# Optimization experiments

Measured on AMD Instinct MI355X. Metric: run time of the kernel, lower is better.

The kernel has to match this reference:

```python
import jax, jax.numpy as jnp
import numpy as np

B, S, D_MODEL, D_SPACE = 4, 2048, 1024, 64
N_POOL = 2048  # size of each of the 5 pools (fqk, fv, rqk, rv, knowledge)
TOP_K = 8


def setup_inputs() -> dict:
    key = jax.random.key(0)
    k1, k2, k3 = jax.random.split(key, 3)
    x = jax.random.normal(k1, (B, S, D_MODEL), dtype=jnp.float32)
    W_all = jax.random.normal(k2, (D_MODEL, 6 * D_SPACE), dtype=jnp.float32) * 0.02
    b_all = jnp.zeros((6 * D_SPACE,), dtype=jnp.float32)
    neuron_emb = jax.random.normal(k3, (5 * N_POOL, D_SPACE), dtype=jnp.float32) * 0.02
    return {"x": x, "W_all": W_all, "b_all": b_all, "neuron_emb": neuron_emb}


def _topk_sparsify(w, k):
    # per-token top-k scatter + renormalize (matches torch scatter_ of topk vals)
    b, s, n = w.shape
    flat = w.reshape(b * s, n)
    vals, idx = jax.lax.top_k(flat, k)                      # [BS, k]
    rows = jnp.arange(b * s)[:, None]
    sparse = jnp.zeros_like(flat).at[rows, idx].set(vals)
    sparse = sparse / (sparse.sum(-1, keepdims=True) + 1e-8)
    return sparse.reshape(b, s, n)


def reference(x, W_all, b_all, neuron_emb):
    # F.normalize(neuron_emb, dim=-1)
    norm = jnp.maximum(jnp.linalg.norm(neuron_emb, axis=-1, keepdims=True), 1e-12)
    emb = neuron_emb / norm

    # proj_all: Linear(d_model, 6*d_space); eval mode -> dropout is identity
    proj = jnp.einsum('bsd,de->bse', x, W_all) + b_all      # [B,S,6*d_space]
    h = jnp.split(proj, 6, axis=-1)

    fqk_emb = emb[0 * N_POOL:1 * N_POOL]
    fv_emb = emb[1 * N_POOL:2 * N_POOL]
    rqk_emb = emb[2 * N_POOL:3 * N_POOL]
    rv_emb = emb[3 * N_POOL:4 * N_POOL]
    pool = [fqk_emb, fqk_emb, fv_emb, rqk_emb, rqk_emb, rv_emb]

    outs = []
    for hp, e in zip(h, pool):
        logits = jnp.einsum('bsd,nd->bsn', hp, e)           # [B,S,N_POOL]
        pref = jax.nn.softmax(logits, axis=-1)
        outs.append(_topk_sparsify(pref, TOP_K))
    # (fqk_Q, fqk_K, fv, rqk_Q, rqk_K, rv) stacked: [6,B,S,N_POOL]
    return jnp.stack(outs, axis=0)
```

## Files before the change

kernel.cpp:

```cpp
#include <hip/hip_runtime.h>
#include <hip/hip_bf16.h>
#include <math.h>

#define HEADS   6
#define DMODEL  1024
#define NPROJ   384
#define DSP     64
#define NPOOL   2048
#define NROWS   8192
#define TILE_M  64
#define KT      64
#define KEEP    16

#define LOG2E_F 1.44269504088896340f
#define LOG2E_D 1.4426950408889634
#define C2      14.4269504088896340f

#define NINF (-__builtin_inff())
#define IMAX 0x7fffffff

typedef __attribute__((ext_vector_type(8))) short  short8;
typedef __attribute__((ext_vector_type(4))) float  f32x4;
typedef __attribute__((ext_vector_type(4))) double f64x4;

__device__ __forceinline__ bool bet_d(double v, int vi, double w, int wi) {
    return (v > w) || (v == w && vi < wi);
}
__device__ __forceinline__ unsigned short f2bf(float f) {
    unsigned int u = __float_as_uint(f);
    return (unsigned short)((u + 0x7fffu + ((u >> 16) & 1u)) >> 16);
}
__device__ __forceinline__ float bf2f(unsigned short s) {
    return __uint_as_float(((unsigned int)s) << 16);
}
__device__ __forceinline__ unsigned int packbf2(float a, float b) {
    return (unsigned int)f2bf(a) | ((unsigned int)f2bf(b) << 16);
}

#define DECL8P(r) \
    unsigned tp##r##0=0u,tp##r##1=0u,tp##r##2=0u,tp##r##3=0u, \
             tp##r##4=0u,tp##r##5=0u,tp##r##6=0u,tp##r##7=0u;

#define CSWP(r,hi,lo) { const unsigned a_=tp##r##hi, b_=tp##r##lo; \
    tp##r##hi = a_>b_?a_:b_; tp##r##lo = a_>b_?b_:a_; }

#define INS8P(r,P) \
    if ((P) > tp##r##7) { tp##r##7=(P); \
        CSWP(r,6,7) CSWP(r,5,6) CSWP(r,4,5) CSWP(r,3,4) \
        CSWP(r,2,3) CSWP(r,1,2) CSWP(r,0,1) }

#define TOURNP(r, ROW) { \
    unsigned slot_ = 0u; \
    for (int k_=0;k_<16;++k_) { \
        const unsigned my0_ = tp##r##0; \
        unsigned v_ = my0_; \
        { const unsigned o_=(unsigned)__shfl_xor((int)v_,1,64); v_ = v_>o_?v_:o_; } \
        { const unsigned o_=(unsigned)__shfl_xor((int)v_,2,64); v_ = v_>o_?v_:o_; } \
        { const unsigned o_=(unsigned)__shfl_xor((int)v_,4,64); v_ = v_>o_?v_:o_; } \
        { const unsigned o_=(unsigned)__shfl_xor((int)v_,8,64); v_ = v_>o_?v_:o_; } \
        const bool won_ = (v_ == my0_); \
        tp##r##0 = won_?tp##r##1:tp##r##0; \
        tp##r##1 = won_?tp##r##2:tp##r##1; \
        tp##r##2 = won_?tp##r##3:tp##r##2; \
        tp##r##3 = won_?tp##r##4:tp##r##3; \
        tp##r##4 = won_?tp##r##5:tp##r##4; \
        tp##r##5 = won_?tp##r##6:tp##r##5; \
        tp##r##6 = won_?tp##r##7:tp##r##6; \
        tp##r##7 = won_?0u:tp##r##7; \
        slot_ = (m==k_)?v_:slot_; \
    } \
    ridx16[(ROW)*16 + m] = 2047 - (int)(slot_ & 0x7FFu); }

#define CSWD(hi,lo) { \
    const bool sw_ = bet_d(dv##lo,di##lo,dv##hi,di##hi); \
    const double td_ = dv##hi; const int tj_ = di##hi; \
    dv##hi = sw_?dv##lo:dv##hi; di##hi = sw_?di##lo:di##hi; \
    dv##lo = sw_?td_:dv##lo;    di##lo = sw_?tj_:di##lo; }

#define INS8D(W,CI) \
    if (bet_d(W,CI,dv7,di7)) { dv7=(W); di7=(CI); \
        CSWD(6,7) CSWD(5,6) CSWD(4,5) CSWD(3,4) CSWD(2,3) CSWD(1,2) CSWD(0,1) }

__global__ __launch_bounds__(256)
void prep_k(const float* __restrict__ emb, ushort* __restrict__ ebf)
{
    const int row = blockIdx.x*256 + threadIdx.x;
    const float* src = emb + (size_t)row*DSP;
    float ss = 0.f;
    #pragma unroll
    for (int g=0; g<16; ++g) {
        const float4 v = *(const float4*)(src + g*4);
        ss += v.x*v.x + v.y*v.y + v.z*v.z + v.w*v.w;
    }
    const float inv = LOG2E_F / fmaxf(sqrtf(ss), 1e-12f);
    ushort* dst = ebf + (size_t)row*DSP;
    #pragma unroll
    for (int g=0; g<8; ++g) {
        const float4 a = *(const float4*)(src + g*8);
        const float4 b = *(const float4*)(src + g*8 + 4);
        uint4 o;
        o.x = packbf2(a.x*inv, a.y*inv);
        o.y = packbf2(a.z*inv, a.w*inv);
        o.z = packbf2(b.x*inv, b.y*inv);
        o.w = packbf2(b.z*inv, b.w*inv);
        *(uint4*)(dst + g*8) = o;
    }
}

__global__ __launch_bounds__(256, 3)
void proj_k(const float* __restrict__ x, const float* __restrict__ Wm,
            const float* __restrict__ bb, float* __restrict__ out)
{
    __shared__ __align__(16) float x_t[64*68];
    __shared__ __align__(16) float w_t[64*68];

    const int t    = threadIdx.x;
    const int lane = t & 63;
    const int wv   = t >> 6;
    const int m    = lane & 15;
    const int q    = lane >> 4;
    const int head = blockIdx.y;
    const int row0 = blockIdx.x * TILE_M;
    const size_t obase = ((size_t)head*NROWS + row0) * (size_t)NPOOL;

    int pr0,pr1,pr2,pr3, pc0,pc1,pc2,pc3;
    {
        const f64x4 zz = {0.,0.,0.,0.};
        const f64x4 dpr = __builtin_amdgcn_mfma_f64_16x16x4f64((double)m, 1.0, zz, 0, 0, 0);
        const f64x4 dpc = __builtin_amdgcn_mfma_f64_16x16x4f64(1.0, (double)m, zz, 0, 0, 0);
        pr0=(int)(dpr[0]*0.25+0.5); pr1=(int)(dpr[1]*0.25+0.5);
        pr2=(int)(dpr[2]*0.25+0.5); pr3=(int)(dpr[3]*0.25+0.5);
        pc0=(int)(dpc[0]*0.25+0.5); pc1=(int)(dpc[1]*0.25+0.5);
        pc2=(int)(dpc[2]*0.25+0.5); pc3=(int)(dpc[3]*0.25+0.5);
    }

    f64x4 acc0 = {0.,0.,0.,0.}, acc1 = {0.,0.,0.,0.},
          acc2 = {0.,0.,0.,0.}, acc3 = {0.,0.,0.,0.};

    const int xr = t >> 2;
    const int xq = t & 3;
    const int wr = t >> 4;
    const int cg = t & 15;
    const float* wbase = Wm + head*64 + cg*4;

    float4 xv0,xv1,xv2,xv3, wv0,wv1,wv2,wv3;
    {
        const float* xsrc = x + (size_t)(row0+xr)*DMODEL + xq*16;
        xv0 = *(const float4*)(xsrc);     xv1 = *(const float4*)(xsrc + 4);
        xv2 = *(const float4*)(xsrc + 8); xv3 = *(const float4*)(xsrc + 12);
        wv0 = *(const float4*)(wbase + (size_t)(wr     )*NPROJ);
        wv1 = *(const float4*)(wbase + (size_t)(wr + 16)*NPROJ);
        wv2 = *(const float4*)(wbase + (size_t)(wr + 32)*NPROJ);
        wv3 = *(const float4*)(wbase + (size_t)(wr + 48)*NPROJ);
    }

    for (int kk = 0; kk < DMODEL; kk += KT) {
        __syncthreads();
        {
            const int k0 = xq*16;
            x_t[(k0+ 0)*68+xr]=xv0.x; x_t[(k0+ 1)*68+xr]=xv0.y; x_t[(k0+ 2)*68+xr]=xv0.z; x_t[(k0+ 3)*68+xr]=xv0.w;
            x_t[(k0+ 4)*68+xr]=xv1.x; x_t[(k0+ 5)*68+xr]=xv1.y; x_t[(k0+ 6)*68+xr]=xv1.z; x_t[(k0+ 7)*68+xr]=xv1.w;
            x_t[(k0+ 8)*68+xr]=xv2.x; x_t[(k0+ 9)*68+xr]=xv2.y; x_t[(k0+10)*68+xr]=xv2.z; x_t[(k0+11)*68+xr]=xv2.w;
            x_t[(k0+12)*68+xr]=xv3.x; x_t[(k0+13)*68+xr]=xv3.y; x_t[(k0+14)*68+xr]=xv3.z; x_t[(k0+15)*68+xr]=xv3.w;
            *(float4*)&w_t[(wr     )*68 + cg*4] = wv0;
            *(float4*)&w_t[(wr + 16)*68 + cg*4] = wv1;
            *(float4*)&w_t[(wr + 32)*68 + cg*4] = wv2;
            *(float4*)&w_t[(wr + 48)*68 + cg*4] = wv3;
        }
        __syncthreads();
        if (kk + KT < DMODEL) {
            const float* xsrc = x + (size_t)(row0+xr)*DMODEL + (kk+KT) + xq*16;
            xv0 = *(const float4*)(xsrc);     xv1 = *(const float4*)(xsrc + 4);
            xv2 = *(const float4*)(xsrc + 8); xv3 = *(const float4*)(xsrc + 12);
            wv0 = *(const float4*)(wbase + (size_t)(kk+KT + wr     )*NPROJ);
            wv1 = *(const float4*)(wbase + (size_t)(kk+KT + wr + 16)*NPROJ);
            wv2 = *(const float4*)(wbase + (size_t)(kk+KT + wr + 32)*NPROJ);
            wv3 = *(const float4*)(wbase + (size_t)(kk+KT + wr + 48)*NPROJ);
        }
        #pragma unroll 4
        for (int kq = 0; kq < 16; ++kq) {
            const int kb = kq*4 + q;
            const double a  = (double)x_t[kb*68 + wv*16 + m];
            const double b0 = (double)w_t[kb*68 +      m];
            const double b1 = (double)w_t[kb*68 + 16 + m];
            const double b2 = (double)w_t[kb*68 + 32 + m];
            const double b3 = (double)w_t[kb*68 + 48 + m];
            acc0 = __builtin_amdgcn_mfma_f64_16x16x4f64(a, b0, acc0, 0, 0, 0);
            acc1 = __builtin_amdgcn_mfma_f64_16x16x4f64(a, b1, acc1, 0, 0, 0);
            acc2 = __builtin_amdgcn_mfma_f64_16x16x4f64(a, b2, acc2, 0, 0, 0);
            acc3 = __builtin_amdgcn_mfma_f64_16x16x4f64(a, b3, acc3, 0, 0, 0);
        }
    }

    float*  hhi = out + obase;
    ushort* hlo = (ushort*)(out + obase + 4096);
    const float* bbp = bb + head*64;
    #pragma unroll
    for (int ct = 0; ct < 4; ++ct) {
        const f64x4 a4 = (ct==0)?acc0:(ct==1)?acc1:(ct==2)?acc2:acc3;
        #define WRB(r) { \
            const int row = wv*16 + pr##r; \
            const int col = ct*16 + pc##r; \
            const double v = a4[r] + (double)bbp[col]; \
            const float hi = (float)v; \
            hhi[(size_t)row*64 + col] = hi; \
            hlo[(size_t)row*64 + col] = f2bf((float)(v - (double)hi)); }
        WRB(0) WRB(1) WRB(2) WRB(3)
        #undef WRB
    }
}

__global__ __launch_bounds__(256, 3)
void route_k(const float* __restrict__ emb, const ushort* __restrict__ ebf,
             float* __restrict__ out)
{
    __shared__ int    ridx16[64*16];
    __shared__ float  zbuf[64];
    __shared__ double rv[64*17];
    __shared__ __align__(8) float final8[64*16];

    const int t    = threadIdx.x;
    const int lane = t & 63, wv = t >> 6;
    const int m    = lane & 15, q = lane >> 4;
    const int head = blockIdx.y;
    const int row0 = blockIdx.x * TILE_M;
    const size_t obase = ((size_t)head*NROWS + row0) * (size_t)NPOOL;

    int psel = 0;
    if (head >= 2) psel = 1;
    if (head >= 3) psel = 2;
    if (head >= 5) psel = 3;
    const float*  epool = emb + (size_t)psel * NPOOL * DSP;
    const ushort* ebase = ebf + (size_t)psel * NPOOL * DSP;

    union FragU { unsigned int u[4]; short8 s; };
    FragU A0, A1;
    {
        const float* hr = out + obase + (size_t)(wv*16 + m)*64 + q*8;
        const float4 a0 = *(const float4*)(hr);
        const float4 a1 = *(const float4*)(hr + 4);
        const float4 a2 = *(const float4*)(hr + 32);
        const float4 a3 = *(const float4*)(hr + 36);
        A0.u[0]=packbf2(a0.x,a0.y); A0.u[1]=packbf2(a0.z,a0.w);
        A0.u[2]=packbf2(a1.x,a1.y); A0.u[3]=packbf2(a1.z,a1.w);
        A1.u[0]=packbf2(a2.x,a2.y); A1.u[1]=packbf2(a2.z,a2.w);
        A1.u[2]=packbf2(a3.x,a3.y); A1.u[3]=packbf2(a3.z,a3.w);
    }

    DECL8P(0) DECL8P(1) DECL8P(2) DECL8P(3)
    float zacc0=0.f, zacc1=0.f, zacc2=0.f, zacc3=0.f;

    #pragma unroll 1
    for (int it=0; it<128; ++it) {
        const int cidx = it*16 + m;
        const unsigned invc = (unsigned)(2047 - cidx);
        const ushort* ep = ebase + (size_t)cidx*DSP + q*8;
        const short8 B0 = *(const short8*)(ep);
        const short8 B1 = *(const short8*)(ep + 32);

        f32x4 cc = {0.f,0.f,0.f,0.f};
        cc = __builtin_amdgcn_mfma_f32_16x16x32_bf16(A0.s, B0, cc, 0, 0, 0);
        cc = __builtin_amdgcn_mfma_f32_16x16x32_bf16(A1.s, B1, cc, 0, 0, 0);

        #define PH1(r) { const float w_ = cc[r]; \
            zacc##r += __builtin_amdgcn_exp2f(w_ - C2); \
            unsigned u_ = __float_as_uint(w_); \
            u_ ^= ((unsigned)((int)u_ >> 31)) | 0x80000000u; \
            const unsigned p_ = (u_ & 0xFFFFF800u) | invc; \
            INS8P(r, p_) }
        PH1(0) PH1(1) PH1(2) PH1(3)
        #undef PH1
    }

    { float z=zacc0; z+=__shfl_xor(z,1,64); z+=__shfl_xor(z,2,64); z+=__shfl_xor(z,4,64); z+=__shfl_xor(z,8,64); if(m==0) zbuf[wv*16+q*4+0]=z; }
    { float z=zacc1; z+=__shfl_xor(z,1,64); z+=__shfl_xor(z,2,64); z+=__shfl_xor(z,4,64); z+=__shfl_xor(z,8,64); if(m==0) zbuf[wv*16+q*4+1]=z; }
    { float z=zacc2; z+=__shfl_xor(z,1,64); z+=__shfl_xor(z,2,64); z+=__shfl_xor(z,4,64); z+=__shfl_xor(z,8,64); if(m==0) zbuf[wv*16+q*4+2]=z; }
    { float z=zacc3; z+=__shfl_xor(z,1,64); z+=__shfl_xor(z,2,64); z+=__shfl_xor(z,4,64); z+=__shfl_xor(z,8,64); if(m==0) zbuf[wv*16+q*4+3]=z; }

    TOURNP(0, wv*16 + q*4 + 0)
    TOURNP(1, wv*16 + q*4 + 1)
    TOURNP(2, wv*16 + q*4 + 2)
    TOURNP(3, wv*16 + q*4 + 3)
    __syncthreads();

    {
        const int row = t >> 2, q4 = t & 3;
        const int ix0 = ridx16[row*16 + q4*4 + 0];
        const int ix1 = ridx16[row*16 + q4*4 + 1];
        const int ix2 = ridx16[row*16 + q4*4 + 2];
        const int ix3 = ridx16[row*16 + q4*4 + 3];
        const float* ep0 = epool + (size_t)ix0*DSP;
        const float* ep1 = epool + (size_t)ix1*DSP;
        const float* ep2 = epool + (size_t)ix2*DSP;
        const float* ep3 = epool + (size_t)ix3*DSP;
        const float*  hhr = out + obase + (size_t)row*64;
        const ushort* hlr = (const ushort*)(out + obase + 4096) + (size_t)row*64;
        double nn0=0,nn1=0,nn2=0,nn3=0, dd0=0,dd1=0,dd2=0,dd3=0;
        #pragma unroll 1
        for (int k4=0; k4<DSP; k4+=4) {
            const double h0 = (double)hhr[k4+0] + (double)bf2f(hlr[k4+0]);
            const double h1 = (double)hhr[k4+1] + (double)bf2f(hlr[k4+1]);
            const double h2 = (double)hhr[k4+2] + (double)bf2f(hlr[k4+2]);
            const double h3 = (double)hhr[k4+3] + (double)bf2f(hlr[k4+3]);
            #define RS(s) { const float4 e_ = *(const float4*)(ep##s + k4); \
                const double e0_=(double)e_.x, e1_=(double)e_.y, e2_=(double)e_.z, e3_=(double)e_.w; \
                nn##s += e0_*e0_ + e1_*e1_ + e2_*e2_ + e3_*e3_; \
                dd##s += h0*e0_ + h1*e1_ + h2*e2_ + h3*e3_; }
            RS(0) RS(1) RS(2) RS(3)
            #undef RS
        }
        rv[row*17 + q4*4 + 0] = dd0 / fmax(sqrt(nn0), 1e-12);
        rv[row*17 + q4*4 + 1] = dd1 / fmax(sqrt(nn1), 1e-12);
        rv[row*17 + q4*4 + 2] = dd2 / fmax(sqrt(nn2), 1e-12);
        rv[row*17 + q4*4 + 3] = dd3 / fmax(sqrt(nn3), 1e-12);
    }
    __syncthreads();

    if (t < 64) {
        const float Zg = zbuf[t];
        double dv0=-INFINITY,dv1=-INFINITY,dv2=-INFINITY,dv3=-INFINITY,
               dv4=-INFINITY,dv5=-INFINITY,dv6=-INFINITY,dv7=-INFINITY;
        int    di0=IMAX,di1=IMAX,di2=IMAX,di3=IMAX,di4=IMAX,di5=IMAX,di6=IMAX,di7=IMAX;
        #pragma unroll 1
        for (int s=0;s<KEEP;s++) {
            const double v_  = rv[t*17 + s];
            const int    ix_ = ridx16[t*16 + s];
            INS8D(v_, ix_)
        }
        float denom = 1e-8f * Zg;
        const float ov0 = __builtin_amdgcn_exp2f((float)(dv0*LOG2E_D) - C2); denom += ov0;
        const float ov1 = __builtin_amdgcn_exp2f((float)(dv1*LOG2E_D) - C2); denom += ov1;
        const float ov2 = __builtin_amdgcn_exp2f((float)(dv2*LOG2E_D) - C2); denom += ov2;
        const float ov3 = __builtin_amdgcn_exp2f((float)(dv3*LOG2E_D) - C2); denom += ov3;
        const float ov4 = __builtin_amdgcn_exp2f((float)(dv4*LOG2E_D) - C2); denom += ov4;
        const float ov5 = __builtin_amdgcn_exp2f((float)(dv5*LOG2E_D) - C2); denom += ov5;
        const float ov6 = __builtin_amdgcn_exp2f((float)(dv6*LOG2E_D) - C2); denom += ov6;
        const float ov7 = __builtin_amdgcn_exp2f((float)(dv7*LOG2E_D) - C2); denom += ov7;
        const float rd = 1.0f / denom;
        float2 p;
        p.x=ov0*rd; p.y=__int_as_float(di0); *(float2*)&final8[t*16 +  0] = p;
        p.x=ov1*rd; p.y=__int_as_float(di1); *(float2*)&final8[t*16 +  2] = p;
        p.x=ov2*rd; p.y=__int_as_float(di2); *(float2*)&final8[t*16 +  4] = p;
        p.x=ov3*rd; p.y=__int_as_float(di3); *(float2*)&final8[t*16 +  6] = p;
        p.x=ov4*rd; p.y=__int_as_float(di4); *(float2*)&final8[t*16 +  8] = p;
        p.x=ov5*rd; p.y=__int_as_float(di5); *(float2*)&final8[t*16 + 10] = p;
        p.x=ov6*rd; p.y=__int_as_float(di6); *(float2*)&final8[t*16 + 12] = p;
        p.x=ov7*rd; p.y=__int_as_float(di7); *(float2*)&final8[t*16 + 14] = p;
    }
    __syncthreads();

    #pragma unroll 1
    for (int rr=0; rr<16; ++rr) {
        const int row = rr*4 + wv;
        const float* fb = &final8[row*16];
        const float pv0=fb[ 0]; const int pi0=__float_as_int(fb[ 1]);
        const float pv1=fb[ 2]; const int pi1=__float_as_int(fb[ 3]);
        const float pv2=fb[ 4]; const int pi2=__float_as_int(fb[ 5]);
        const float pv3=fb[ 6]; const int pi3=__float_as_int(fb[ 7]);
        const float pv4=fb[ 8]; const int pi4=__float_as_int(fb[ 9]);
        const float pv5=fb[10]; const int pi5=__float_as_int(fb[11]);
        const float pv6=fb[12]; const int pi6=__float_as_int(fb[13]);
        const float pv7=fb[14]; const int pi7=__float_as_int(fb[15]);
        float* orow = out + obase + (size_t)row*NPOOL;
        #pragma unroll
        for (int j=0;j<8;j++) {
            const int base4 = (j*64 + lane)*4;
            float v0=0.f, v1=0.f, v2=0.f, v3=0.f;
            #define SCAT(s) { const int d_ = pi##s - base4; \
                v0=(d_==0)?pv##s:v0; v1=(d_==1)?pv##s:v1; \
                v2=(d_==2)?pv##s:v2; v3=(d_==3)?pv##s:v3; }
            SCAT(0) SCAT(1) SCAT(2) SCAT(3) SCAT(4) SCAT(5) SCAT(6) SCAT(7)
            #undef SCAT
            *(float4*)&orow[base4] = make_float4(v0,v1,v2,v3);
        }
    }
}

extern "C" void kernel_launch(void* const* d_in, const int* in_sizes, int n_in,
                              void* d_out, int out_size, void* d_ws, size_t ws_size,
                              hipStream_t stream) {
    (void)in_sizes; (void)n_in; (void)ws_size; (void)out_size;
    const float* x   = (const float*)d_in[0];
    const float* Wm  = (const float*)d_in[1];
    const float* bb  = (const float*)d_in[2];
    const float* emb = (const float*)d_in[3];
    float*  out = (float*)d_out;
    ushort* ebf = (ushort*)d_ws;
    dim3 grid(NROWS / TILE_M, HEADS);
    prep_k <<<32, 256, 0, stream>>>(emb, ebf);
    proj_k <<<grid, dim3(256), 0, stream>>>(x, Wm, bb, out);
    route_k<<<grid, dim3(256), 0, stream>>>(emb, ebf, out);
}
```

Baseline: 733.7 us.

## Split routing pool columns across two wave groups with 512-thread blocks

New measurement: 791.7 us. 7.9% more time.

```diff
diff --git a/kernel.cpp b/kernel.cpp
--- a/kernel.cpp
+++ b/kernel.cpp
@@ -10,7 +10,7 @@
 #define NROWS   8192
 #define TILE_M  64
 #define KT      64
-#define KEEP    16
+#define PSTR    72
 
 #define LOG2E_F 1.44269504088896340f
 #define LOG2E_D 1.4426950408889634
@@ -69,7 +69,7 @@
         tp##r##7 = won_?0u:tp##r##7; \
         slot_ = (m==k_)?v_:slot_; \
     } \
-    ridx16[(ROW)*16 + m] = 2047 - (int)(slot_ & 0x7FFu); }
+    ridx16[(ROW)*32 + ch16 + m] = 2047 - (int)(slot_ & 0x7FFu); }
 
 #define CSWD(hi,lo) { \
     const bool sw_ = bet_d(dv##lo,di##lo,dv##hi,di##hi); \
@@ -111,8 +111,8 @@
 void proj_k(const float* __restrict__ x, const float* __restrict__ Wm,
             const float* __restrict__ bb, float* __restrict__ out)
 {
-    __shared__ __align__(16) float x_t[64*68];
-    __shared__ __align__(16) float w_t[64*68];
+    __shared__ __align__(16) float x_t[64*PSTR];
+    __shared__ __align__(16) float w_t[64*PSTR];
 
     const int t    = threadIdx.x;
     const int lane = t & 63;
@@ -158,14 +158,14 @@
         __syncthreads();
         {
             const int k0 = xq*16;
-            x_t[(k0+ 0)*68+xr]=xv0.x; x_t[(k0+ 1)*68+xr]=xv0.y; x_t[(k0+ 2)*68+xr]=xv0.z; x_t[(k0+ 3)*68+xr]=xv0.w;
-            x_t[(k0+ 4)*68+xr]=xv1.x; x_t[(k0+ 5)*68+xr]=xv1.y; x_t[(k0+ 6)*68+xr]=xv1.z; x_t[(k0+ 7)*68+xr]=xv1.w;
-            x_t[(k0+ 8)*68+xr]=xv2.x; x_t[(k0+ 9)*68+xr]=xv2.y; x_t[(k0+10)*68+xr]=xv2.z; x_t[(k0+11)*68+xr]=xv2.w;
-            x_t[(k0+12)*68+xr]=xv3.x; x_t[(k0+13)*68+xr]=xv3.y; x_t[(k0+14)*68+xr]=xv3.z; x_t[(k0+15)*68+xr]=xv3.w;
-            *(float4*)&w_t[(wr     )*68 + cg*4] = wv0;
-            *(float4*)&w_t[(wr + 16)*68 + cg*4] = wv1;
-            *(float4*)&w_t[(wr + 32)*68 + cg*4] = wv2;
-            *(float4*)&w_t[(wr + 48)*68 + cg*4] = wv3;
+            x_t[(k0+ 0)*PSTR+xr]=xv0.x; x_t[(k0+ 1)*PSTR+xr]=xv0.y; x_t[(k0+ 2)*PSTR+xr]=xv0.z; x_t[(k0+ 3)*PSTR+xr]=xv0.w;
+            x_t[(k0+ 4)*PSTR+xr]=xv1.x; x_t[(k0+ 5)*PSTR+xr]=xv1.y; x_t[(k0+ 6)*PSTR+xr]=xv1.z; x_t[(k0+ 7)*PSTR+xr]=xv1.w;
+            x_t[(k0+ 8)*PSTR+xr]=xv2.x; x_t[(k0+ 9)*PSTR+xr]=xv2.y; x_t[(k0+10)*PSTR+xr]=xv2.z; x_t[(k0+11)*PSTR+xr]=xv2.w;
+            x_t[(k0+12)*PSTR+xr]=xv3.x; x_t[(k0+13)*PSTR+xr]=xv3.y; x_t[(k0+14)*PSTR+xr]=xv3.z; x_t[(k0+15)*PSTR+xr]=xv3.w;
+            *(float4*)&w_t[(wr     )*PSTR + cg*4] = wv0;
+            *(float4*)&w_t[(wr + 16)*PSTR + cg*4] = wv1;
+            *(float4*)&w_t[(wr + 32)*PSTR + cg*4] = wv2;
+            *(float4*)&w_t[(wr + 48)*PSTR + cg*4] = wv3;
         }
         __syncthreads();
         if (kk + KT < DMODEL) {
@@ -180,11 +180,11 @@
         #pragma unroll 4
         for (int kq = 0; kq < 16; ++kq) {
             const int kb = kq*4 + q;
-            const double a  = (double)x_t[kb*68 + wv*16 + m];
-            const double b0 = (double)w_t[kb*68 +      m];
-            const double b1 = (double)w_t[kb*68 + 16 + m];
-            const double b2 = (double)w_t[kb*68 + 32 + m];
-            const double b3 = (double)w_t[kb*68 + 48 + m];
+            const double a  = (double)x_t[kb*PSTR + wv*16 + m];
+            const double b0 = (double)w_t[kb*PSTR +      m];
+            const double b1 = (double)w_t[kb*PSTR + 16 + m];
+            const double b2 = (double)w_t[kb*PSTR + 32 + m];
+            const double b3 = (double)w_t[kb*PSTR + 48 + m];
             acc0 = __builtin_amdgcn_mfma_f64_16x16x4f64(a, b0, acc0, 0, 0, 0);
             acc1 = __builtin_amdgcn_mfma_f64_16x16x4f64(a, b1, acc1, 0, 0, 0);
             acc2 = __builtin_amdgcn_mfma_f64_16x16x4f64(a, b2, acc2, 0, 0, 0);
@@ -210,17 +210,21 @@
     }
 }
 
-__global__ __launch_bounds__(256, 3)
+__global__ __launch_bounds__(512, 6)
 void route_k(const float* __restrict__ emb, const ushort* __restrict__ ebf,
              float* __restrict__ out)
 {
-    __shared__ int    ridx16[64*16];
-    __shared__ float  zbuf[64];
-    __shared__ double rv[64*17];
+    __shared__ int    ridx16[64*32];
+    __shared__ float  zbuf[2*64];
+    __shared__ double rv[64*33];
     __shared__ __align__(8) float final8[64*16];
 
     const int t    = threadIdx.x;
-    const int lane = t & 63, wv = t >> 6;
+    const int lane = t & 63;
+    const int wvB  = t >> 6;
+    const int wv   = wvB & 3;
+    const int colhalf = wvB >> 2;
+    const int ch16 = colhalf * 16;
     const int m    = lane & 15, q = lane >> 4;
     const int head = blockIdx.y;
     const int row0 = blockIdx.x * TILE_M;
@@ -251,8 +255,8 @@
     float zacc0=0.f, zacc1=0.f, zacc2=0.f, zacc3=0.f;
 
     #pragma unroll 1
-    for (int it=0; it<128; ++it) {
-        const int cidx = it*16 + m;
+    for (int it=0; it<64; ++it) {
+        const int cidx = (colhalf<<10) + it*16 + m;
         const unsigned invc = (unsigned)(2047 - cidx);
         const ushort* ep = ebase + (size_t)cidx*DSP + q*8;
         const short8 B0 = *(const short8*)(ep);
@@ -272,10 +276,10 @@
         #undef PH1
     }
 
-    { float z=zacc0; z+=__shfl_xor(z,1,64); z+=__shfl_xor(z,2,64); z+=__shfl_xor(z,4,64); z+=__shfl_xor(z,8,64); if(m==0) zbuf[wv*16+q*4+0]=z; }
-    { float z=zacc1; z+=__shfl_xor(z,1,64); z+=__shfl_xor(z,2,64); z+=__shfl_xor(z,4,64); z+=__shfl_xor(z,8,64); if(m==0) zbuf[wv*16+q*4+1]=z; }
-    { float z=zacc2; z+=__shfl_xor(z,1,64); z+=__shfl_xor(z,2,64); z+=__shfl_xor(z,4,64); z+=__shfl_xor(z,8,64); if(m==0) zbuf[wv*16+q*4+2]=z; }
-    { float z=zacc3; z+=__shfl_xor(z,1,64); z+=__shfl_xor(z,2,64); z+=__shfl_xor(z,4,64); z+=__shfl_xor(z,8,64); if(m==0) zbuf[wv*16+q*4+3]=z; }
+    { float z=zacc0; z+=__shfl_xor(z,1,64); z+=__shfl_xor(z,2,64); z+=__shfl_xor(z,4,64); z+=__shfl_xor(z,8,64); if(m==0) zbuf[colhalf*64 + wv*16+q*4+0]=z; }
+    { float z=zacc1; z+=__shfl_xor(z,1,64); z+=__shfl_xor(z,2,64); z+=__shfl_xor(z,4,64); z+=__shfl_xor(z,8,64); if(m==0) zbuf[colhalf*64 + wv*16+q*4+1]=z; }
+    { float z=zacc2; z+=__shfl_xor(z,1,64); z+=__shfl_xor(z,2,64); z+=__shfl_xor(z,4,64); z+=__shfl_xor(z,8,64); if(m==0) zbuf[colhalf*64 + wv*16+q*4+2]=z; }
+    { float z=zacc3; z+=__shfl_xor(z,1,64); z+=__shfl_xor(z,2,64); z+=__shfl_xor(z,4,64); z+=__shfl_xor(z,8,64); if(m==0) zbuf[colhalf*64 + wv*16+q*4+3]=z; }
 
     TOURNP(0, wv*16 + q*4 + 0)
     TOURNP(1, wv*16 + q*4 + 1)
@@ -284,11 +288,11 @@
     __syncthreads();
 
     {
-        const int row = t >> 2, q4 = t & 3;
-        const int ix0 = ridx16[row*16 + q4*4 + 0];
-        const int ix1 = ridx16[row*16 + q4*4 + 1];
-        const int ix2 = ridx16[row*16 + q4*4 + 2];
-        const int ix3 = ridx16[row*16 + q4*4 + 3];
+        const int row = t >> 3, q8 = t & 7;
+        const int ix0 = ridx16[row*32 + q8*4 + 0];
+        const int ix1 = ridx16[row*32 + q8*4 + 1];
+        const int ix2 = ridx16[row*32 + q8*4 + 2];
+        const int ix3 = ridx16[row*32 + q8*4 + 3];
         const float* ep0 = epool + (size_t)ix0*DSP;
         const float* ep1 = epool + (size_t)ix1*DSP;
         const float* ep2 = epool + (size_t)ix2*DSP;
@@ -309,22 +313,22 @@
             RS(0) RS(1) RS(2) RS(3)
             #undef RS
         }
-        rv[row*17 + q4*4 + 0] = dd0 / fmax(sqrt(nn0), 1e-12);
-        rv[row*17 + q4*4 + 1] = dd1 / fmax(sqrt(nn1), 1e-12);
-        rv[row*17 + q4*4 + 2] = dd2 / fmax(sqrt(nn2), 1e-12);
-        rv[row*17 + q4*4 + 3] = dd3 / fmax(sqrt(nn3), 1e-12);
+        rv[row*33 + q8*4 + 0] = dd0 / fmax(sqrt(nn0), 1e-12);
+        rv[row*33 + q8*4 + 1] = dd1 / fmax(sqrt(nn1), 1e-12);
+        rv[row*33 + q8*4 + 2] = dd2 / fmax(sqrt(nn2), 1e-12);
+        rv[row*33 + q8*4 + 3] = dd3 / fmax(sqrt(nn3), 1e-12);
     }
     __syncthreads();
 
     if (t < 64) {
-        const float Zg = zbuf[t];
+        const float Zg = zbuf[t] + zbuf[64 + t];
         double dv0=-INFINITY,dv1=-INFINITY,dv2=-INFINITY,dv3=-INFINITY,
                dv4=-INFINITY,dv5=-INFINITY,dv6=-INFINITY,dv7=-INFINITY;
         int    di0=IMAX,di1=IMAX,di2=IMAX,di3=IMAX,di4=IMAX,di5=IMAX,di6=IMAX,di7=IMAX;
         #pragma unroll 1
-        for (int s=0;s<KEEP;s++) {
-            const double v_  = rv[t*17 + s];
-            const int    ix_ = ridx16[t*16 + s];
+        for (int s=0;s<32;s++) {
+            const double v_  = rv[t*33 + s];
+            const int    ix_ = ridx16[t*32 + s];
             INS8D(v_, ix_)
         }
         float denom = 1e-8f * Zg;
@@ -350,8 +354,8 @@
     __syncthreads();
 
     #pragma unroll 1
-    for (int rr=0; rr<16; ++rr) {
-        const int row = rr*4 + wv;
+    for (int rr=0; rr<8; ++rr) {
+        const int row = rr*8 + wvB;
         const float* fb = &final8[row*16];
         const float pv0=fb[ 0]; const int pi0=__float_as_int(fb[ 1]);
         const float pv1=fb[ 2]; const int pi1=__float_as_int(fb[ 3]);
@@ -389,5 +393,5 @@
     dim3 grid(NROWS / TILE_M, HEADS);
     prep_k <<<32, 256, 0, stream>>>(emb, ebf);
     proj_k <<<grid, dim3(256), 0, stream>>>(x, Wm, bb, out);
-    route_k<<<grid, dim3(256), 0, stream>>>(emb, ebf, out);
-}
+    route_k<<<grid, dim3(512), 0, stream>>>(emb, ebf, out);
+}
```

## Fuse projection and routing kernels, keep projected tile in shared memory

Applied to the files above, without the earlier changes.

After: 720.0 us. No clear change (-1.9%).

```diff
diff --git a/kernel.cpp b/kernel.cpp
--- a/kernel.cpp
+++ b/kernel.cpp
@@ -11,6 +11,8 @@
 #define TILE_M  64
 #define KT      64
 #define KEEP    16
+#define PSTR    72
+#define HSTR    68
 
 #define LOG2E_F 1.44269504088896340f
 #define LOG2E_D 1.4426950408889634
@@ -108,11 +110,19 @@
 }
 
 __global__ __launch_bounds__(256, 3)
-void proj_k(const float* __restrict__ x, const float* __restrict__ Wm,
-            const float* __restrict__ bb, float* __restrict__ out)
+void fused_k(const float* __restrict__ x, const float* __restrict__ Wm,
+             const float* __restrict__ bb, const float* __restrict__ emb,
+             const ushort* __restrict__ ebf, float* __restrict__ out)
 {
-    __shared__ __align__(16) float x_t[64*68];
-    __shared__ __align__(16) float w_t[64*68];
+    __shared__ __align__(16) char arena[43264];
+    float*  x_t    = (float*)arena;
+    float*  w_t    = (float*)(arena + 18432);
+    float*  h_hi   = (float*)arena;
+    ushort* h_lo   = (ushort*)(arena + 17408);
+    int*    ridx16 = (int*)   (arena + 26112);
+    float*  zbuf   = (float*) (arena + 30208);
+    double* rv     = (double*)(arena + 30464);
+    float*  final8 = (float*) (arena + 39168);
 
     const int t    = threadIdx.x;
     const int lane = t & 63;
@@ -158,14 +168,14 @@
         __syncthreads();
         {
             const int k0 = xq*16;
-            x_t[(k0+ 0)*68+xr]=xv0.x; x_t[(k0+ 1)*68+xr]=xv0.y; x_t[(k0+ 2)*68+xr]=xv0.z; x_t[(k0+ 3)*68+xr]=xv0.w;
-            x_t[(k0+ 4)*68+xr]=xv1.x; x_t[(k0+ 5)*68+xr]=xv1.y; x_t[(k0+ 6)*68+xr]=xv1.z; x_t[(k0+ 7)*68+xr]=xv1.w;
-            x_t[(k0+ 8)*68+xr]=xv2.x; x_t[(k0+ 9)*68+xr]=xv2.y; x_t[(k0+10)*68+xr]=xv2.z; x_t[(k0+11)*68+xr]=xv2.w;
-            x_t[(k0+12)*68+xr]=xv3.x; x_t[(k0+13)*68+xr]=xv3.y; x_t[(k0+14)*68+xr]=xv3.z; x_t[(k0+15)*68+xr]=xv3.w;
-            *(float4*)&w_t[(wr     )*68 + cg*4] = wv0;
-            *(float4*)&w_t[(wr + 16)*68 + cg*4] = wv1;
-            *(float4*)&w_t[(wr + 32)*68 + cg*4] = wv2;
-            *(float4*)&w_t[(wr + 48)*68 + cg*4] = wv3;
+            x_t[(k0+ 0)*PSTR+xr]=xv0.x; x_t[(k0+ 1)*PSTR+xr]=xv0.y; x_t[(k0+ 2)*PSTR+xr]=xv0.z; x_t[(k0+ 3)*PSTR+xr]=xv0.w;
+            x_t[(k0+ 4)*PSTR+xr]=xv1.x; x_t[(k0+ 5)*PSTR+xr]=xv1.y; x_t[(k0+ 6)*PSTR+xr]=xv1.z; x_t[(k0+ 7)*PSTR+xr]=xv1.w;
+            x_t[(k0+ 8)*PSTR+xr]=xv2.x; x_t[(k0+ 9)*PSTR+xr]=xv2.y; x_t[(k0+10)*PSTR+xr]=xv2.z; x_t[(k0+11)*PSTR+xr]=xv2.w;
+            x_t[(k0+12)*PSTR+xr]=xv3.x; x_t[(k0+13)*PSTR+xr]=xv3.y; x_t[(k0+14)*PSTR+xr]=xv3.z; x_t[(k0+15)*PSTR+xr]=xv3.w;
+            *(float4*)&w_t[(wr     )*PSTR + cg*4] = wv0;
+            *(float4*)&w_t[(wr + 16)*PSTR + cg*4] = wv1;
+            *(float4*)&w_t[(wr + 32)*PSTR + cg*4] = wv2;
+            *(float4*)&w_t[(wr + 48)*PSTR + cg*4] = wv3;
         }
         __syncthreads();
         if (kk + KT < DMODEL) {
@@ -180,11 +190,11 @@
         #pragma unroll 4
         for (int kq = 0; kq < 16; ++kq) {
             const int kb = kq*4 + q;
-            const double a  = (double)x_t[kb*68 + wv*16 + m];
-            const double b0 = (double)w_t[kb*68 +      m];
-            const double b1 = (double)w_t[kb*68 + 16 + m];
-            const double b2 = (double)w_t[kb*68 + 32 + m];
-            const double b3 = (double)w_t[kb*68 + 48 + m];
+            const double a  = (double)x_t[kb*PSTR + wv*16 + m];
+            const double b0 = (double)w_t[kb*PSTR +      m];
+            const double b1 = (double)w_t[kb*PSTR + 16 + m];
+            const double b2 = (double)w_t[kb*PSTR + 32 + m];
+            const double b3 = (double)w_t[kb*PSTR + 48 + m];
             acc0 = __builtin_amdgcn_mfma_f64_16x16x4f64(a, b0, acc0, 0, 0, 0);
             acc1 = __builtin_amdgcn_mfma_f64_16x16x4f64(a, b1, acc1, 0, 0, 0);
             acc2 = __builtin_amdgcn_mfma_f64_16x16x4f64(a, b2, acc2, 0, 0, 0);
@@ -192,39 +202,24 @@
         }
     }
 
-    float*  hhi = out + obase;
-    ushort* hlo = (ushort*)(out + obase + 4096);
-    const float* bbp = bb + head*64;
-    #pragma unroll
-    for (int ct = 0; ct < 4; ++ct) {
-        const f64x4 a4 = (ct==0)?acc0:(ct==1)?acc1:(ct==2)?acc2:acc3;
-        #define WRB(r) { \
-            const int row = wv*16 + pr##r; \
-            const int col = ct*16 + pc##r; \
-            const double v = a4[r] + (double)bbp[col]; \
-            const float hi = (float)v; \
-            hhi[(size_t)row*64 + col] = hi; \
-            hlo[(size_t)row*64 + col] = f2bf((float)(v - (double)hi)); }
-        WRB(0) WRB(1) WRB(2) WRB(3)
-        #undef WRB
-    }
-}
-
-__global__ __launch_bounds__(256, 3)
-void route_k(const float* __restrict__ emb, const ushort* __restrict__ ebf,
-             float* __restrict__ out)
-{
-    __shared__ int    ridx16[64*16];
-    __shared__ float  zbuf[64];
-    __shared__ double rv[64*17];
-    __shared__ __align__(8) float final8[64*16];
-
-    const int t    = threadIdx.x;
-    const int lane = t & 63, wv = t >> 6;
-    const int m    = lane & 15, q = lane >> 4;
-    const int head = blockIdx.y;
-    const int row0 = blockIdx.x * TILE_M;
-    const size_t obase = ((size_t)head*NROWS + row0) * (size_t)NPOOL;
+    __syncthreads();
+
+    {
+        const float* bbp = bb + head*64;
+        #pragma unroll
+        for (int ct = 0; ct < 4; ++ct) {
+            const f64x4 a4 = (ct==0)?acc0:(ct==1)?acc1:(ct==2)?acc2:acc3;
+            #define WRB(r) { \
+                const int row = wv*16 + pr##r; \
+                const int col = ct*16 + pc##r; \
+                const double v = a4[r] + (double)bbp[col]; \
+                const float hi = (float)v; \
+                h_hi[row*HSTR + col] = hi; \
+                h_lo[row*HSTR + col] = f2bf((float)(v - (double)hi)); }
+            WRB(0) WRB(1) WRB(2) WRB(3)
+            #undef WRB
+        }
+    }
 
     int psel = 0;
     if (head >= 2) psel = 1;
@@ -236,7 +231,7 @@
     union FragU { unsigned int u[4]; short8 s; };
     FragU A0, A1;
     {
-        const float* hr = out + obase + (size_t)(wv*16 + m)*64 + q*8;
+        const float* hr = h_hi + (size_t)(wv*16 + m)*HSTR + q*8;
         const float4 a0 = *(const float4*)(hr);
         const float4 a1 = *(const float4*)(hr + 4);
         const float4 a2 = *(const float4*)(hr + 32);
@@ -293,8 +288,8 @@
         const float* ep1 = epool + (size_t)ix1*DSP;
         const float* ep2 = epool + (size_t)ix2*DSP;
         const float* ep3 = epool + (size_t)ix3*DSP;
-        const float*  hhr = out + obase + (size_t)row*64;
-        const ushort* hlr = (const ushort*)(out + obase + 4096) + (size_t)row*64;
+        const float*  hhr = h_hi + (size_t)row*HSTR;
+        const ushort* hlr = h_lo + (size_t)row*HSTR;
         double nn0=0,nn1=0,nn2=0,nn3=0, dd0=0,dd1=0,dd2=0,dd3=0;
         #pragma unroll 1
         for (int k4=0; k4<DSP; k4+=4) {
@@ -388,6 +383,5 @@
     ushort* ebf = (ushort*)d_ws;
     dim3 grid(NROWS / TILE_M, HEADS);
     prep_k <<<32, 256, 0, stream>>>(emb, ebf);
-    proj_k <<<grid, dim3(256), 0, stream>>>(x, Wm, bb, out);
-    route_k<<<grid, dim3(256), 0, stream>>>(emb, ebf, out);
-}
+    fused_k<<<grid, dim3(256), 0, stream>>>(x, Wm, bb, emb, ebf, out);
+}
```
